# Kernel optimization log

Hardware: AMD Instinct MI355X
Metric: run time of the kernel (lower is better)

The kernel has to match this reference:

```python
import jax, jax.numpy as jnp
import numpy as np

B, C_IN, T, H, W = 32, 1024, 7, 14, 14
C_INTER = 512


def setup_inputs() -> dict:
    key = jax.random.key(0)
    ks = jax.random.split(key, 8)
    s = lambda fan_in: 1.0 / np.sqrt(fan_in)
    return {
        "x_window": jax.random.normal(ks[0], (B, C_IN, T, H, W), jnp.float32),
        "nodes": jax.random.normal(ks[1], (T, C_INTER), jnp.float32),
        "Wq": jax.random.normal(ks[2], (C_IN, C_INTER), jnp.float32) * s(C_IN),
        "bq": jnp.zeros((C_INTER,), jnp.float32),
        "Wk": jax.random.normal(ks[3], (C_INTER, C_INTER), jnp.float32) * s(C_INTER),
        "bk": jnp.zeros((C_INTER,), jnp.float32),
        "Wv": jax.random.normal(ks[4], (C_IN, C_INTER), jnp.float32) * s(C_IN),
        "bv": jnp.zeros((C_INTER,), jnp.float32),
        "Wo": jax.random.normal(ks[5], (C_INTER, C_IN), jnp.float32) * s(C_INTER),
        "bo": jnp.zeros((C_IN,), jnp.float32),
    }


def reference(x_window, nodes, Wq, bq, Wk, bk, Wv, bv, Wo, bo):
    # x_window: (B, C_in, T, H, W); dropout is identity at eval time.
    t_mid = x_window.shape[2] // 2
    x_item = x_window[:, :, t_mid]                                   # (B, C_in, H, W)
    # pointwise (Linear3d) projections over channel dim
    query = jnp.einsum("bchw,cd->bdhw", x_item, Wq) + bq[None, :, None, None]
    key = nodes @ Wk + bk                                            # (T, C_inter)
    value = jnp.einsum("bcthw,cd->bdthw", x_window, Wv) + bv[None, :, None, None, None]
    # per-pixel attention scores over the T node keys
    alpha = jnp.einsum("bdhw,td->bthw", query, key)                  # (B, T, H, W)
    alpha = jax.nn.softmax(alpha, axis=1)
    # per-pixel weighted temporal sum
    y = jnp.einsum("bthw,bdthw->bdhw", alpha, value)                 # (B, C_inter, H, W)
    out = jnp.einsum("bdhw,dc->bchw", y, Wo) + bo[None, :, None, None]
    return out[:, :, None]                                           # (B, C_in, 1, H, W)
```

## Files before the change

kernel.cpp:

```cpp
#include <hip/hip_runtime.h>
#include <hip/hip_bf16.h>
#include <stdint.h>

#define BB    32
#define CIN   1024
#define TT    7
#define HHWW  196
#define HW4   49
#define CI    512
#define TMID  3
#define MM    (BB*HHWW)
#define NCH   16
#define CSZ   64

using bf16 = __hip_bfloat16;
typedef __attribute__((ext_vector_type(8))) short short8;
typedef __attribute__((ext_vector_type(4))) short s16x4;
typedef __attribute__((ext_vector_type(4))) float f32x4;

__device__ __forceinline__ void gload_lds16(const void* g, void* l) {
    __builtin_amdgcn_global_load_lds((const __attribute__((address_space(1))) void*)g,
                                     (__attribute__((address_space(3))) void*)l, 16, 0, 0);
}

template <int EPI>
__device__ __forceinline__ void gemm_body(const bf16* __restrict__ A, const bf16* __restrict__ Bt,
                                          void* __restrict__ Cout, const float* __restrict__ bias,
                                          int M, int N, int K, int bm, int bn,
                                          bf16* As, bf16* Bs) {
    int tid = threadIdx.x;
    int wid = tid >> 6, lane = tid & 63;
    int wr = wid >> 1, wc = wid & 1;
    f32x4 acc[4][4] = {};
    const bf16* Ab = A + (size_t)bm * 128 * K;
    const bf16* Bb = Bt + (size_t)bn * 128 * K;
    int row = lane & 15;
    int kb_base = (lane >> 4) * 8;

    auto stage = [&](int buf, int k0) {
        #pragma unroll
        for (int it = 0; it < 4; ++it) {
            int e = (it * 256 + tid) * 8;
            int r = e >> 6, cc = e & 63;
            gload_lds16(Ab + (size_t)r * K + k0 + cc, &As[buf * 8192 + e]);
            gload_lds16(Bb + (size_t)r * K + k0 + cc, &Bs[buf * 8192 + e]);
        }
    };

    stage(0, 0);
    int cur = 0;
    for (int k0 = 0; k0 < K; k0 += 64) {
        __syncthreads();
        if (k0 + 64 < K) stage(cur ^ 1, k0 + 64);
        bf16* Ac = &As[cur * 8192];
        bf16* Bc = &Bs[cur * 8192];
        #pragma unroll
        for (int kk = 0; kk < 2; ++kk) {
            int kb = kk * 32 + kb_base;
            short8 a[4], b[4];
            #pragma unroll
            for (int mi = 0; mi < 4; ++mi) a[mi] = *(const short8*)&Ac[(wr * 64 + mi * 16 + row) * 64 + kb];
            #pragma unroll
            for (int ni = 0; ni < 4; ++ni) b[ni] = *(const short8*)&Bc[(wc * 64 + ni * 16 + row) * 64 + kb];
            #pragma unroll
            for (int mi = 0; mi < 4; ++mi)
                #pragma unroll
                for (int ni = 0; ni < 4; ++ni)
                    acc[mi][ni] = __builtin_amdgcn_mfma_f32_16x16x32_bf16(a[mi], b[ni], acc[mi][ni], 0, 0, 0);
        }
        cur ^= 1;
    }

    int col_l = lane & 15, row_l = (lane >> 4) * 4;
    if constexpr (EPI == 0) {
        bf16* C = (bf16*)Cout;
        #pragma unroll
        for (int mi = 0; mi < 4; ++mi) {
            int row0 = bm * 128 + wr * 64 + mi * 16 + row_l;
            #pragma unroll
            for (int ni = 0; ni < 4; ++ni) {
                int col = bn * 128 + wc * 64 + ni * 16 + col_l;
                #pragma unroll
                for (int r = 0; r < 4; ++r)
                    C[(size_t)(row0 + r) * N + col] = __float2bfloat16(acc[mi][ni][r]);
            }
        }
    } else {
        float* Cf = (float*)Cout;
        #pragma unroll
        for (int ni = 0; ni < 4; ++ni) {
            int n = bn * 128 + wc * 64 + ni * 16 + col_l;
            float bz = bias[n];
            #pragma unroll
            for (int mi = 0; mi < 4; ++mi) {
                int m0 = bm * 128 + wr * 64 + mi * 16 + row_l;
                int b = m0 / HHWW;
                int hw0 = m0 - b * HHWW;
                f32x4 v = acc[mi][ni];
                v[0] += bz; v[1] += bz; v[2] += bz; v[3] += bz;
                *(f32x4*)&Cf[((size_t)b * CIN + n) * HHWW + hw0] = v;
            }
        }
    }
}

__global__ __launch_bounds__(256) void k_prep1(
    const float* __restrict__ nodes, const float* __restrict__ Wk, const float* __restrict__ bk,
    float* __restrict__ key,
    const float* __restrict__ Wv, const float* __restrict__ Wo,
    bf16* __restrict__ Wv_bf, bf16* __restrict__ WoT_bf,
    const float* __restrict__ bv, const float* __restrict__ bo, float* __restrict__ bvo) {
    __shared__ float sred[256];
    int u = blockIdx.x, tid = threadIdx.x;
    if (u < 56) {
        int t = u >> 3, dc = u & 7;
        int d_l = tid & 63, q = tid >> 6;
        int d = dc * 64 + d_l;
        float acc = 0.f;
        const float* nr = nodes + t * CI;
        #pragma unroll 4
        for (int c = q * 128; c < q * 128 + 128; ++c)
            acc = fmaf(nr[c], Wk[(size_t)c * CI + d], acc);
        sred[q * 64 + d_l] = acc;
        __syncthreads();
        if (q == 0)
            key[t * CI + d] = sred[d_l] + sred[64 + d_l] + sred[128 + d_l] + sred[192 + d_l] + bk[d];
    } else if (u < 56 + 2048) {
        int i = (u - 56) * 256 + tid;
        Wv_bf[i] = __float2bfloat16(Wv[i]);
        int d = i >> 10, cp = i & 1023;
        WoT_bf[(size_t)cp * CI + d] = __float2bfloat16(Wo[i]);
    } else {
        int cp0 = (u - 2104) * 32;
        int cp_l = tid & 31, dq = tid >> 5;
        float acc = 0.f;
        #pragma unroll 4
        for (int d = dq * 64; d < dq * 64 + 64; ++d)
            acc = fmaf(bv[d], Wo[(size_t)d * CIN + cp0 + cp_l], acc);
        sred[dq * 32 + cp_l] = acc;
        __syncthreads();
        if (dq == 0) {
            float v = bo[cp0 + cp_l];
            #pragma unroll
            for (int g = 0; g < 8; ++g) v += sred[g * 32 + cp_l];
            bvo[cp0 + cp_l] = v;
        }
    }
}

__global__ __launch_bounds__(256) void k_prep2(
    const bf16* __restrict__ WoT_bf, const bf16* __restrict__ Wv_bf, bf16* __restrict__ WvoT,
    const float* __restrict__ Wq, const float* __restrict__ bq,
    const float* __restrict__ key, float* __restrict__ Wqk, float* __restrict__ bqk) {
    __shared__ __align__(16) bf16 As[2 * 128 * 64];
    __shared__ __align__(16) bf16 Bs[2 * 128 * 64];
    int bid = blockIdx.x;
    if (bid < 64) {
        gemm_body<0>(WoT_bf, Wv_bf, (void*)WvoT, nullptr, 1024, 1024, 512, bid >> 3, bid & 7, As, Bs);
        return;
    }
    int c = (bid - 64) * 4 + (threadIdx.x >> 6);
    int lane = threadIdx.x & 63;
    if (c > CIN) return;
    const float* src = (c < CIN) ? (Wq + (size_t)c * CI) : bq;
    float acc[TT] = {};
    #pragma unroll 2
    for (int it = 0; it < CI / 64; ++it) {
        float w = src[it * 64 + lane];
        #pragma unroll
        for (int t = 0; t < TT; ++t) acc[t] = fmaf(w, key[t * CI + it * 64 + lane], acc[t]);
    }
    #pragma unroll
    for (int t = 0; t < TT; ++t) {
        float v = acc[t];
        for (int off = 32; off; off >>= 1) v += __shfl_down(v, off);
        if (lane == 0) { if (c < CIN) Wqk[c * 8 + t] = v; else bqk[t] = v; }
    }
}

__global__ __launch_bounds__(256) void k_alpha(const float* __restrict__ x,
                                               const float* __restrict__ Wqk,
                                               float* __restrict__ part) {
    __shared__ float wq_s[CSZ * 8];
    int ch = blockIdx.x, b = blockIdx.y;
    int tid = threadIdx.x;
    for (int i = tid; i < CSZ * 8; i += 256) wq_s[i] = Wqk[ch * CSZ * 8 + i];
    __syncthreads();
    if (tid < HHWW) {
        float acc[TT] = {};
        const float* xb = x + (size_t)(b * CIN + ch * CSZ) * TT * HHWW + TMID * HHWW + tid;
        #pragma unroll 8
        for (int c = 0; c < CSZ; ++c) {
            float v = xb[(size_t)c * TT * HHWW];
            #pragma unroll
            for (int t = 0; t < TT; ++t) acc[t] = fmaf(v, wq_s[c * 8 + t], acc[t]);
        }
        #pragma unroll
        for (int t = 0; t < TT; ++t)
            part[((size_t)(b * NCH + ch) * TT + t) * HHWW + tid] = acc[t];
    }
}

__global__ __launch_bounds__(256) void k_softmaxF(const float* __restrict__ part,
                                                  const float* __restrict__ bqk,
                                                  float* __restrict__ alphaF) {
    int b = blockIdx.x;
    int tid = threadIdx.x;
    if (tid >= HHWW) return;
    float s[TT];
    #pragma unroll
    for (int t = 0; t < TT; ++t) s[t] = bqk[t];
    #pragma unroll
    for (int ch = 0; ch < NCH; ++ch)
        #pragma unroll
        for (int t = 0; t < TT; ++t)
            s[t] += part[((size_t)(b * NCH + ch) * TT + t) * HHWW + tid];
    float mx = s[0];
    #pragma unroll
    for (int t = 1; t < TT; ++t) mx = fmaxf(mx, s[t]);
    float e[TT], sum = 0.f;
    #pragma unroll
    for (int t = 0; t < TT; ++t) { e[t] = __expf(s[t] - mx); sum += e[t]; }
    float inv = 1.f / sum;
    #pragma unroll
    for (int t = 0; t < TT; ++t) alphaF[(size_t)b * TT * HHWW + t * HHWW + tid] = e[t] * inv;
}

__global__ __launch_bounds__(256) void k_smxw(const float* __restrict__ x,
                                              const float* __restrict__ alphaF,
                                              bf16* __restrict__ xw) {
    __shared__ __align__(16) float al[TT * HHWW];
    __shared__ __align__(16) bf16 txp[HHWW * 32];
    int c0 = blockIdx.x * 32;
    int b = blockIdx.y;
    int tid = threadIdx.x;
    for (int i = tid; i < TT * HHWW; i += 256) al[i] = alphaF[(size_t)b * TT * HHWW + i];
    __syncthreads();
    const f32x4* xp = (const f32x4*)x;
    f32x4 acc[7] = {};
    #pragma unroll
    for (int t = 0; t < TT; ++t) {
        #pragma unroll
        for (int k = 0; k < 7; ++k) {
            int w = k * 256 + tid;
            if (k == 6 && w >= 1568) continue;
            int c_l = w / 49;
            int hw4 = w - c_l * 49;
            f32x4 a4 = *(const f32x4*)&al[t * HHWW + hw4 * 4];
            f32x4 xv = xp[((size_t)(b * CIN + c0 + c_l) * TT + t) * HW4 + hw4];
            acc[k] += a4 * xv;
        }
    }
    #pragma unroll
    for (int k = 0; k < 7; ++k) {
        int w = k * 256 + tid;
        if (k == 6 && w >= 1568) continue;
        int c_l = w / 49;
        int hw4 = w - c_l * 49;
        int v = (hw4 & 7) << 2;
        #pragma unroll
        for (int r = 0; r < 4; ++r)
            txp[(hw4 * 4 + r) * 32 + (c_l ^ v)] = __float2bfloat16(acc[k][r]);
    }
    __syncthreads();
    #pragma unroll
    for (int k = 0; k < 7; ++k) {
        int w = k * 256 + tid;
        if (k == 6 && w >= 1568) continue;
        int m = w >> 3, seg = w & 7;
        int v = ((m >> 2) & 7) << 2;
        s16x4 val = *(const s16x4*)&txp[m * 32 + ((seg * 4) ^ v)];
        *(s16x4*)&xw[(size_t)(b * HHWW + m) * CIN + c0 + seg * 4] = val;
    }
}

__global__ __launch_bounds__(256) void k_gemm1(const bf16* __restrict__ A, const bf16* __restrict__ Bt,
                                               float* __restrict__ C, const float* __restrict__ bias) {
    __shared__ __align__(16) bf16 As[2 * 128 * 64];
    __shared__ __align__(16) bf16 Bs[2 * 128 * 64];
    gemm_body<1>(A, Bt, (void*)C, bias, MM, CIN, CIN, blockIdx.x, blockIdx.y, As, Bs);
}

extern "C" void kernel_launch(void* const* d_in, const int* in_sizes, int n_in,
                              void* d_out, int out_size, void* d_ws, size_t ws_size,
                              hipStream_t stream) {
    const float* x     = (const float*)d_in[0];
    const float* nodes = (const float*)d_in[1];
    const float* Wq    = (const float*)d_in[2];
    const float* bq    = (const float*)d_in[3];
    const float* Wk    = (const float*)d_in[4];
    const float* bk    = (const float*)d_in[5];
    const float* Wv    = (const float*)d_in[6];
    const float* bv    = (const float*)d_in[7];
    const float* Wo    = (const float*)d_in[8];
    const float* bo    = (const float*)d_in[9];

    uint8_t* w = (uint8_t*)d_ws;
    size_t off = 0;
    auto alloc = [&](size_t bytes) -> void* {
        void* p = w + off;
        off = (off + bytes + 255) & ~(size_t)255;
        return p;
    };
    float* key    = (float*)alloc((size_t)TT * CI * 4);
    float* Wqk    = (float*)alloc((size_t)CIN * 8 * 4);
    float* bqk    = (float*)alloc(8 * 4);
    float* bvo    = (float*)alloc((size_t)CIN * 4);
    bf16*  Wv_bf  = (bf16*)alloc((size_t)CIN * CI * 2);
    bf16*  WoT_bf = (bf16*)alloc((size_t)CIN * CI * 2);
    bf16*  WvoT   = (bf16*)alloc((size_t)CIN * CIN * 2);
    float* part   = (float*)alloc((size_t)BB * NCH * TT * HHWW * 4);
    float* alphaF = (float*)alloc((size_t)BB * TT * HHWW * 4);
    bf16*  xw     = (bf16*)alloc((size_t)MM * CIN * 2);
    (void)ws_size;

    k_prep1<<<2136, 256, 0, stream>>>(nodes, Wk, bk, key, Wv, Wo, Wv_bf, WoT_bf, bv, bo, bvo);
    k_prep2<<<321, 256, 0, stream>>>(WoT_bf, Wv_bf, WvoT, Wq, bq, key, Wqk, bqk);
    k_alpha<<<dim3(NCH, BB), 256, 0, stream>>>(x, Wqk, part);
    k_softmaxF<<<BB, 256, 0, stream>>>(part, bqk, alphaF);
    k_smxw<<<dim3(32, BB), 256, 0, stream>>>(x, alphaF, xw);
    k_gemm1<<<dim3(49, 8), 256, 0, stream>>>(xw, WvoT, (float*)d_out, bvo);
}
```

Before: 98.53 us.

## Fuse softmax into alpha kernel via counter, tile Wo transpose, remap GEMM blocks

The softmax kernel is folded into k_alpha: the last channel-chunk block for each batch, found through an atomic counter, does the reduction and softmax, which removes one launch. In k_prep1 the weight conversion is vectorised to 4-wide, and the Wo transpose now goes through an LDS tile so global writes are coalesced, which shrinks the grid from 2136 to 728 blocks. The GEMM launch becomes a 1D grid with a block-index remap meant to improve L2 reuse. The counters are zeroed in k_prep1, which makes the kernels depend on launch order and adds an atomic and fence per block.

Result: slower. 117.1 us (+18.9%).

```diff
diff --git a/kernel.cpp b/kernel.cpp
--- a/kernel.cpp
+++ b/kernel.cpp
@@ -21,6 +21,10 @@
 __device__ __forceinline__ void gload_lds16(const void* g, void* l) {
     __builtin_amdgcn_global_load_lds((const __attribute__((address_space(1))) void*)g,
                                      (__attribute__((address_space(3))) void*)l, 16, 0, 0);
+}
+
+__device__ __forceinline__ int ctr_inc_acqrel(int* p) {
+    return __hip_atomic_fetch_add(p, 1, __ATOMIC_ACQ_REL, __HIP_MEMORY_SCOPE_AGENT);
 }
 
 template <int EPI>
@@ -109,9 +113,11 @@
     float* __restrict__ key,
     const float* __restrict__ Wv, const float* __restrict__ Wo,
     bf16* __restrict__ Wv_bf, bf16* __restrict__ WoT_bf,
-    const float* __restrict__ bv, const float* __restrict__ bo, float* __restrict__ bvo) {
-    __shared__ float sred[256];
+    const float* __restrict__ bv, const float* __restrict__ bo, float* __restrict__ bvo,
+    int* __restrict__ ctr) {
+    __shared__ __align__(16) float lds[64 * 65];
     int u = blockIdx.x, tid = threadIdx.x;
+    if (u == 0 && tid < 32) ctr[tid] = 0;
     if (u < 56) {
         int t = u >> 3, dc = u & 7;
         int d_l = tid & 63, q = tid >> 6;
@@ -121,28 +127,45 @@
         #pragma unroll 4
         for (int c = q * 128; c < q * 128 + 128; ++c)
             acc = fmaf(nr[c], Wk[(size_t)c * CI + d], acc);
-        sred[q * 64 + d_l] = acc;
+        lds[q * 64 + d_l] = acc;
         __syncthreads();
         if (q == 0)
-            key[t * CI + d] = sred[d_l] + sred[64 + d_l] + sred[128 + d_l] + sred[192 + d_l] + bk[d];
-    } else if (u < 56 + 2048) {
-        int i = (u - 56) * 256 + tid;
-        Wv_bf[i] = __float2bfloat16(Wv[i]);
-        int d = i >> 10, cp = i & 1023;
-        WoT_bf[(size_t)cp * CI + d] = __float2bfloat16(Wo[i]);
+            key[t * CI + d] = lds[d_l] + lds[64 + d_l] + lds[128 + d_l] + lds[192 + d_l] + bk[d];
+    } else if (u < 568) {
+        int i4 = ((u - 56) * 256 + tid) * 4;
+        f32x4 v = *(const f32x4*)&Wv[i4];
+        s16x4 o;
+        #pragma unroll
+        for (int j = 0; j < 4; ++j) { bf16 h = __float2bfloat16(v[j]); o[j] = *(short*)&h; }
+        *(s16x4*)&Wv_bf[i4] = o;
+    } else if (u < 696) {
+        int u3 = u - 568;
+        int dt = u3 >> 4, ct = u3 & 15;
+        int r0 = tid >> 6, c = tid & 63;
+        #pragma unroll
+        for (int k = 0; k < 16; ++k) {
+            int r = k * 4 + r0;
+            lds[r * 65 + c] = Wo[(size_t)(dt * 64 + r) * CIN + ct * 64 + c];
+        }
+        __syncthreads();
+        #pragma unroll
+        for (int k = 0; k < 16; ++k) {
+            int r = k * 4 + r0;
+            WoT_bf[(size_t)(ct * 64 + r) * CI + dt * 64 + c] = __float2bfloat16(lds[c * 65 + r]);
+        }
     } else {
-        int cp0 = (u - 2104) * 32;
+        int cp0 = (u - 696) * 32;
         int cp_l = tid & 31, dq = tid >> 5;
         float acc = 0.f;
         #pragma unroll 4
         for (int d = dq * 64; d < dq * 64 + 64; ++d)
             acc = fmaf(bv[d], Wo[(size_t)d * CIN + cp0 + cp_l], acc);
-        sred[dq * 32 + cp_l] = acc;
+        lds[dq * 32 + cp_l] = acc;
         __syncthreads();
         if (dq == 0) {
             float v = bo[cp0 + cp_l];
             #pragma unroll
-            for (int g = 0; g < 8; ++g) v += sred[g * 32 + cp_l];
+            for (int g = 0; g < 8; ++g) v += lds[g * 32 + cp_l];
             bvo[cp0 + cp_l] = v;
         }
     }
@@ -180,8 +203,12 @@
 
 __global__ __launch_bounds__(256) void k_alpha(const float* __restrict__ x,
                                                const float* __restrict__ Wqk,
-                                               float* __restrict__ part) {
+                                               float* __restrict__ part,
+                                               const float* __restrict__ bqk,
+                                               float* __restrict__ alphaF,
+                                               int* __restrict__ ctr) {
     __shared__ float wq_s[CSZ * 8];
+    __shared__ int sflag;
     int ch = blockIdx.x, b = blockIdx.y;
     int tid = threadIdx.x;
     for (int i = tid; i < CSZ * 8; i += 256) wq_s[i] = Wqk[ch * CSZ * 8 + i];
@@ -199,31 +226,31 @@
         for (int t = 0; t < TT; ++t)
             part[((size_t)(b * NCH + ch) * TT + t) * HHWW + tid] = acc[t];
     }
-}
-
-__global__ __launch_bounds__(256) void k_softmaxF(const float* __restrict__ part,
-                                                  const float* __restrict__ bqk,
-                                                  float* __restrict__ alphaF) {
-    int b = blockIdx.x;
-    int tid = threadIdx.x;
-    if (tid >= HHWW) return;
-    float s[TT];
-    #pragma unroll
-    for (int t = 0; t < TT; ++t) s[t] = bqk[t];
-    #pragma unroll
-    for (int ch = 0; ch < NCH; ++ch)
-        #pragma unroll
-        for (int t = 0; t < TT; ++t)
-            s[t] += part[((size_t)(b * NCH + ch) * TT + t) * HHWW + tid];
-    float mx = s[0];
-    #pragma unroll
-    for (int t = 1; t < TT; ++t) mx = fmaxf(mx, s[t]);
-    float e[TT], sum = 0.f;
-    #pragma unroll
-    for (int t = 0; t < TT; ++t) { e[t] = __expf(s[t] - mx); sum += e[t]; }
-    float inv = 1.f / sum;
-    #pragma unroll
-    for (int t = 0; t < TT; ++t) alphaF[(size_t)b * TT * HHWW + t * HHWW + tid] = e[t] * inv;
+    __syncthreads();
+    if (tid == 0) {
+        __threadfence();
+        sflag = (ctr_inc_acqrel(&ctr[b]) == NCH - 1);
+    }
+    __syncthreads();
+    if (sflag && tid < HHWW) {
+        float s[TT];
+        #pragma unroll
+        for (int t = 0; t < TT; ++t) s[t] = bqk[t];
+        #pragma unroll
+        for (int c2 = 0; c2 < NCH; ++c2)
+            #pragma unroll
+            for (int t = 0; t < TT; ++t)
+                s[t] += part[((size_t)(b * NCH + c2) * TT + t) * HHWW + tid];
+        float mx = s[0];
+        #pragma unroll
+        for (int t = 1; t < TT; ++t) mx = fmaxf(mx, s[t]);
+        float e[TT], sum = 0.f;
+        #pragma unroll
+        for (int t = 0; t < TT; ++t) { e[t] = __expf(s[t] - mx); sum += e[t]; }
+        float inv = 1.f / sum;
+        #pragma unroll
+        for (int t = 0; t < TT; ++t) alphaF[(size_t)b * TT * HHWW + t * HHWW + tid] = e[t] * inv;
+    }
 }
 
 __global__ __launch_bounds__(256) void k_smxw(const float* __restrict__ x,
@@ -278,7 +305,10 @@
                                                float* __restrict__ C, const float* __restrict__ bias) {
     __shared__ __align__(16) bf16 As[2 * 128 * 64];
     __shared__ __align__(16) bf16 Bs[2 * 128 * 64];
-    gemm_body<1>(A, Bt, (void*)C, bias, MM, CIN, CIN, blockIdx.x, blockIdx.y, As, Bs);
+    int id = blockIdx.x;
+    int wg = (id & 7) * 49 + (id >> 3);
+    int bm = wg >> 3, bn = wg & 7;
+    gemm_body<1>(A, Bt, (void*)C, bias, MM, CIN, CIN, bm, bn, As, Bs);
 }
 
 extern "C" void kernel_launch(void* const* d_in, const int* in_sizes, int n_in,
@@ -312,12 +342,12 @@
     float* part   = (float*)alloc((size_t)BB * NCH * TT * HHWW * 4);
     float* alphaF = (float*)alloc((size_t)BB * TT * HHWW * 4);
     bf16*  xw     = (bf16*)alloc((size_t)MM * CIN * 2);
+    int*   ctr    = (int*)alloc(64 * 4);
     (void)ws_size;
 
-    k_prep1<<<2136, 256, 0, stream>>>(nodes, Wk, bk, key, Wv, Wo, Wv_bf, WoT_bf, bv, bo, bvo);
+    k_prep1<<<728, 256, 0, stream>>>(nodes, Wk, bk, key, Wv, Wo, Wv_bf, WoT_bf, bv, bo, bvo, ctr);
     k_prep2<<<321, 256, 0, stream>>>(WoT_bf, Wv_bf, WvoT, Wq, bq, key, Wqk, bqk);
-    k_alpha<<<dim3(NCH, BB), 256, 0, stream>>>(x, Wqk, part);
-    k_softmaxF<<<BB, 256, 0, stream>>>(part, bqk, alphaF);
+    k_alpha<<<dim3(NCH, BB), 256, 0, stream>>>(x, Wqk, part, bqk, alphaF, ctr);
     k_smxw<<<dim3(32, BB), 256, 0, stream>>>(x, alphaF, xw);
-    k_gemm1<<<dim3(49, 8), 256, 0, stream>>>(xw, WvoT, (float*)d_out, bvo);
-}
+    k_gemm1<<<392, 256, 0, stream>>>(xw, WvoT, (float*)d_out, bvo);
+}
```
